# Kernel tuning notes

Measured on AMD Instinct MI355X. Metric: run time of the kernel, lower is better.

## Reference

```python
import jax, jax.numpy as jnp
import numpy as np

B, L, D = 8, 4096, 1024


def setup_inputs() -> dict:
    key = jax.random.key(0)
    k1, k2, k3 = jax.random.split(key, 3)
    scale = 1.0 / np.sqrt(D)  # ~xavier magnitude for DxD
    return {
        "x": jax.random.normal(k1, (B, L, D), dtype=jnp.float32),
        "hidden": jnp.zeros((B, D), dtype=jnp.float32),
        "Wg": jax.random.normal(k2, (D, D), dtype=jnp.float32) * scale,
        "bg": jnp.ones((D,), dtype=jnp.float32),  # gate bias init = 1.0
        "Wh": jax.random.normal(k3, (D, D), dtype=jnp.float32) * scale,
        "bh": jnp.zeros((D,), dtype=jnp.float32),
    }


def reference(x, hidden, Wg, bg, Wh, bh):
    # g_t = sigmoid(x W_g^T + b_g); c_t = tanh(x W_h^T + b_h)
    g = jax.nn.sigmoid(jnp.einsum('bld,ed->ble', x, Wg) + bg)
    c = jnp.tanh(jnp.einsum('bld,ed->ble', x, Wh) + bh)
    # linear recurrence h_t = a_t * h_{t-1} + b_t with a=g, b=(1-g)*c
    a = g
    b = (1.0 - g) * c

    def combine(left, right):
        al, bl = left
        ar, br = right
        return ar * al, ar * bl + br

    A, Bv = jax.lax.associative_scan(combine, (a, b), axis=1)
    # h_t = A_t * h0 + B_t  (cumulative affine map applied to init hidden)
    return A * hidden[:, None, :] + Bv
```

## Files before the change

### kernel.cpp

```cpp
#include <hip/hip_runtime.h>
#include <hip/hip_bf16.h>
#include <cstdint>


using u16   = unsigned short;
using f32x4 = __attribute__((ext_vector_type(4))) float;
using h16x4 = __attribute__((ext_vector_type(4))) _Float16;
using h16x8 = __attribute__((ext_vector_type(8))) _Float16;

#define M_TOTAL 32768
#define K_DIM   1024
#define E_DIM   1024
#define LCH     32
#define NCH     128

__global__ void prep(const float* __restrict__ x,
                     const float* __restrict__ wg, const float* __restrict__ wh,
                     u16* __restrict__ x16, u16* __restrict__ wg16,
                     u16* __restrict__ wh16) {
    const size_t XQ = (size_t)M_TOTAL * K_DIM / 4;
    const size_t WQ = (size_t)K_DIM * E_DIM / 4;
    size_t i = (size_t)blockIdx.x * 256 + threadIdx.x;
    const float* src;
    u16* dst;
    size_t j;
    if (i < XQ)           { src = x;  dst = x16;  j = i; }
    else if (i < XQ + WQ) { src = wg; dst = wg16; j = i - XQ; }
    else                  { src = wh; dst = wh16; j = i - XQ - WQ; }
    f32x4 f = ((const f32x4*)src)[j];
    h16x4 h;
#pragma unroll
    for (int c = 0; c < 4; ++c) h[c] = (_Float16)f[c];
    ((h16x4*)dst)[j] = h;
}

__device__ inline float fast_sigmoid(float z) {
    return 1.f / (1.f + __expf(-z));
}
__device__ inline float fast_tanh(float z) {
    return 1.f - 2.f / (__expf(2.f * z) + 1.f);
}

__global__ __launch_bounds__(512, 4) void gemm_act(
    const u16* __restrict__ x16,
    const u16* __restrict__ wg_h, const u16* __restrict__ wh_h,
    const float* __restrict__ bg, const float* __restrict__ bh,
    _Float16* __restrict__ g_out, _Float16* __restrict__ c_out,
    float* __restrict__ Ac, float* __restrict__ Bc) {

    const int bid   = blockIdx.x;
    const int xcd   = bid & 7;
    const int local = bid >> 3;
    const int mt    = xcd * 32 + (local >> 3);
    const int et    = local & 7;
    const int e0    = et * 128;
    const int m0    = mt * 128;

    __shared__ __align__(16) union SM {
        struct {
            u16 A[512 * 8];
            u16 B[2][512 * 8];
        } buf[2];
        struct {
            float g[32][132];
            float c[32][132];
        } ep;
    } sm;

    const int tid  = threadIdx.x;
    const int lane = tid & 63;
    const int wave = tid >> 6;
    const int wr = wave >> 2, wc = wave & 3;
    const int lr = lane & 15;
    const int kg = lane >> 4;

    const int sp   = tid >> 3;
    const int sc   = tid & 7;
    const int sclog = sc ^ (sp & 7);
    const int srow  = sp * 2 + (sclog >> 2);
    const int skc   = sclog & 3;
    const u16* aSrc = x16 + (size_t)(m0 + srow) * K_DIM + skc * 8;
    const u16* bgSrc = wg_h + (size_t)(e0 + srow) * K_DIM + skc * 8;
    const u16* bhSrc = wh_h + (size_t)(e0 + srow) * K_DIM + skc * 8;

    int aoff[4], boff[2];
#pragma unroll
    for (int tr = 0; tr < 4; ++tr) {
        int r = wr * 64 + tr * 16 + lr;
        int p = r >> 1;
        int c = (((r & 1) << 2) | kg) ^ (p & 7);
        aoff[tr] = p * 64 + c * 8;
    }
#pragma unroll
    for (int tc = 0; tc < 2; ++tc) {
        int e = wc * 32 + tc * 16 + lr;
        int p = e >> 1;
        int c = (((e & 1) << 2) | kg) ^ (p & 7);
        boff[tc] = p * 64 + c * 8;
    }

    f32x4 accg[4][2], acch[4][2];
#pragma unroll
    for (int tr = 0; tr < 4; ++tr)
#pragma unroll
        for (int tc = 0; tc < 2; ++tc) {
            accg[tr][tc] = (f32x4){0.f, 0.f, 0.f, 0.f};
            acch[tr][tc] = (f32x4){0.f, 0.f, 0.f, 0.f};
        }

#define STAGE(bi, kt)                                                          \
    do {                                                                       \
        size_t ko = (size_t)(kt) * 32;                                         \
        __builtin_amdgcn_global_load_lds(                                      \
            (const __attribute__((address_space(1))) void*)(aSrc + ko),        \
            (__attribute__((address_space(3))) void*)(&sm.buf[bi].A[tid * 8]), \
            16, 0, 0);                                                         \
        __builtin_amdgcn_global_load_lds(                                      \
            (const __attribute__((address_space(1))) void*)(bgSrc + ko),       \
            (__attribute__((address_space(3))) void*)(&sm.buf[bi].B[0][tid * 8]),\
            16, 0, 0);                                                         \
        __builtin_amdgcn_global_load_lds(                                      \
            (const __attribute__((address_space(1))) void*)(bhSrc + ko),       \
            (__attribute__((address_space(3))) void*)(&sm.buf[bi].B[1][tid * 8]),\
            16, 0, 0);                                                         \
    } while (0)

    STAGE(0, 0);
    __syncthreads();

    int cur = 0;
    for (int kt = 0; kt < K_DIM / 32; ++kt) {
        if (kt + 1 < K_DIM / 32) STAGE(cur ^ 1, kt + 1);

        const u16* Ab  = sm.buf[cur].A;
        const u16* Bg  = sm.buf[cur].B[0];
        const u16* Bh  = sm.buf[cur].B[1];

        h16x8 ah[4];
#pragma unroll
        for (int tr = 0; tr < 4; ++tr)
            ah[tr] = *(const h16x8*)&Ab[aoff[tr]];
#pragma unroll
        for (int tc = 0; tc < 2; ++tc) {
            h16x8 bgv = *(const h16x8*)&Bg[boff[tc]];
            h16x8 bhv = *(const h16x8*)&Bh[boff[tc]];
#pragma unroll
            for (int tr = 0; tr < 4; ++tr) {
                accg[tr][tc] = __builtin_amdgcn_mfma_f32_16x16x32_f16(ah[tr], bgv, accg[tr][tc], 0, 0, 0);
                acch[tr][tc] = __builtin_amdgcn_mfma_f32_16x16x32_f16(ah[tr], bhv, acch[tr][tc], 0, 0, 0);
            }
        }

        __syncthreads();
        cur ^= 1;
    }
#undef STAGE

    float bgv[2], bhv[2];
#pragma unroll
    for (int tc = 0; tc < 2; ++tc) {
        int el = e0 + wc * 32 + tc * 16 + lr;
        bgv[tc] = bg[el];
        bhv[tc] = bh[el];
    }

#pragma unroll
    for (int s = 0; s < 4; ++s) {
        __syncthreads();
        if (wr == (s >> 1)) {
#pragma unroll
            for (int half = 0; half < 2; ++half) {
                int tr = (s & 1) * 2 + half;
#pragma unroll
                for (int tc = 0; tc < 2; ++tc) {
                    int el = wc * 32 + tc * 16 + lr;
#pragma unroll
                    for (int i = 0; i < 4; ++i) {
                        int row = half * 16 + kg * 4 + i;
                        sm.ep.g[row][el] = fast_sigmoid(accg[tr][tc][i] + bgv[tc]);
                        sm.ep.c[row][el] = fast_tanh(acch[tr][tc][i] + bhv[tc]);
                    }
                }
            }
        }
        __syncthreads();

        {
            int row = tid >> 4;
            int c8  = (tid & 15) * 8;
            size_t gofs = (size_t)(m0 + s * 32 + row) * E_DIM + e0 + c8;
            f32x4 v0 = *(const f32x4*)&sm.ep.g[row][c8];
            f32x4 v1 = *(const f32x4*)&sm.ep.g[row][c8 + 4];
            h16x8 hv;
#pragma unroll
            for (int j = 0; j < 4; ++j) { hv[j] = (_Float16)v0[j]; hv[j + 4] = (_Float16)v1[j]; }
            *(h16x8*)(g_out + gofs) = hv;
            v0 = *(const f32x4*)&sm.ep.c[row][c8];
            v1 = *(const f32x4*)&sm.ep.c[row][c8 + 4];
#pragma unroll
            for (int j = 0; j < 4; ++j) { hv[j] = (_Float16)v0[j]; hv[j + 4] = (_Float16)v1[j]; }
            *(h16x8*)(c_out + gofs) = hv;
        }

        if (tid < 128) {
            float A = 1.f, Bv = 0.f;
#pragma unroll 8
            for (int t = 0; t < LCH; ++t) {
                float g = (float)(_Float16)sm.ep.g[t][tid];
                float c = (float)(_Float16)sm.ep.c[t][tid];
                A  = g * A;
                Bv = g * Bv + (1.f - g) * c;
            }
            int m_abs = m0 + s * 32;
            int b  = m_abs >> 12;
            int ch = (m_abs & 4095) >> 5;
            size_t o = ((size_t)b * NCH + ch) * 1024 + e0 + tid;
            Ac[o] = A;
            Bc[o] = Bv;
        }
    }
}

__global__ void chunk_prefix(const float* __restrict__ Ac, const float* __restrict__ Bc,
                             const float* __restrict__ hidden, float* __restrict__ Hst) {
    int idx = blockIdx.x * 256 + threadIdx.x;
    int b = idx >> 10;
    int d = idx & 1023;
    float h = hidden[b * 1024 + d];
#pragma unroll 8
    for (int ch = 0; ch < NCH; ++ch) {
        size_t o = ((size_t)b * NCH + ch) * 1024 + d;
        float A = Ac[o], Bv = Bc[o];
        Hst[o] = h;
        h = A * h + Bv;
    }
}

__global__ void chunk_apply(const _Float16* __restrict__ g_arr,
                            const _Float16* __restrict__ c_arr,
                            const float* __restrict__ Hst,
                            float* __restrict__ out) {
    int d8 = threadIdx.x * 8;
    int ch = blockIdx.x;
    int b  = blockIdx.y;
    size_t base = ((size_t)b * 4096 + (size_t)ch * LCH) * 1024 + d8;
    size_t ho = ((size_t)b * NCH + ch) * 1024 + d8;
    f32x4 h0 = *(const f32x4*)(Hst + ho);
    f32x4 h1 = *(const f32x4*)(Hst + ho + 4);
    float h[8] = {h0[0], h0[1], h0[2], h0[3], h1[0], h1[1], h1[2], h1[3]};
#pragma unroll 4
    for (int t = 0; t < LCH; ++t) {
        size_t idx = base + (size_t)t * 1024;
        h16x8 gv = *(const h16x8*)(g_arr + idx);
        h16x8 cv = *(const h16x8*)(c_arr + idx);
#pragma unroll
        for (int j = 0; j < 8; ++j) {
            float g = (float)gv[j];
            float c = (float)cv[j];
            h[j] = g * h[j] + (1.f - g) * c;
        }
        *(f32x4*)(out + idx)     = (f32x4){h[0], h[1], h[2], h[3]};
        *(f32x4*)(out + idx + 4) = (f32x4){h[4], h[5], h[6], h[7]};
    }
}

extern "C" void kernel_launch(void* const* d_in, const int* in_sizes, int n_in,
                              void* d_out, int out_size, void* d_ws, size_t ws_size,
                              hipStream_t stream) {
    const float* x      = (const float*)d_in[0];
    const float* hidden = (const float*)d_in[1];
    const float* Wg     = (const float*)d_in[2];
    const float* bg     = (const float*)d_in[3];
    const float* Wh     = (const float*)d_in[4];
    const float* bh     = (const float*)d_in[5];
    float* out = (float*)d_out;

    char* ws = (char*)d_ws;
    const size_t WSEG = 2u * 1024u * 1024u;
    u16* wg_h = (u16*)(ws + 0 * WSEG);
    u16* wh_h = (u16*)(ws + 1 * WSEG);
    const size_t HBYTES = (size_t)M_TOTAL * E_DIM * 2;
    _Float16* g_arr = (_Float16*)(ws + 4 * WSEG);
    _Float16* c_arr = (_Float16*)(ws + 4 * WSEG + HBYTES);
    const size_t SSEG = (size_t)8 * NCH * 1024 * 4;
    float* Ac  = (float*)(ws + 4 * WSEG + 2 * HBYTES);
    float* Bc  = (float*)(ws + 4 * WSEG + 2 * HBYTES + SSEG);
    float* Hst = (float*)(ws + 4 * WSEG + 2 * HBYTES + 2 * SSEG);

    u16* x16 = (u16*)d_out;

    const int XQ = M_TOTAL * (K_DIM / 4);
    const int WQ = K_DIM * (E_DIM / 4);
    prep<<<dim3((XQ + 2 * WQ) / 256), 256, 0, stream>>>(x, Wg, Wh, x16, wg_h, wh_h);

    gemm_act<<<dim3(2048), 512, 0, stream>>>(
        x16, wg_h, wh_h, bg, bh, g_arr, c_arr, Ac, Bc);

    chunk_prefix<<<dim3(32), 256, 0, stream>>>(Ac, Bc, hidden, Hst);
    chunk_apply<<<dim3(NCH, 8), 128, 0, stream>>>(g_arr, c_arr, Hst, out);
}
```

Before: 458.1 us.

## Load GEMM B operands directly from global, grid-stride prep, wider chunk_apply blocks

The GEMM kernel stops staging the Wg/Wh weight tiles through LDS and has each lane load its B fragments straight from global memory every k-step, keeping only the x tile double-buffered in LDS. The aim is to cut LDS traffic and footprint so more blocks fit per CU. The prep conversion kernel becomes a grid-stride loop over 2048 blocks, and chunk_apply handles two chunks per 256-thread block. The risk is that the direct global weight loads are uncoalesced, sit on the critical path without prefetch, and are re-read by every wave instead of being shared through LDS.

```diff
diff --git a/kernel.cpp b/kernel.cpp
--- a/kernel.cpp
+++ b/kernel.cpp
@@ -20,18 +20,21 @@
                      u16* __restrict__ wh16) {
     const size_t XQ = (size_t)M_TOTAL * K_DIM / 4;
     const size_t WQ = (size_t)K_DIM * E_DIM / 4;
-    size_t i = (size_t)blockIdx.x * 256 + threadIdx.x;
-    const float* src;
-    u16* dst;
-    size_t j;
-    if (i < XQ)           { src = x;  dst = x16;  j = i; }
-    else if (i < XQ + WQ) { src = wg; dst = wg16; j = i - XQ; }
-    else                  { src = wh; dst = wh16; j = i - XQ - WQ; }
-    f32x4 f = ((const f32x4*)src)[j];
-    h16x4 h;
-#pragma unroll
-    for (int c = 0; c < 4; ++c) h[c] = (_Float16)f[c];
-    ((h16x4*)dst)[j] = h;
+    const size_t TOT = XQ + 2 * WQ;
+    for (size_t i = (size_t)blockIdx.x * 256 + threadIdx.x; i < TOT;
+         i += (size_t)2048 * 256) {
+        const float* src;
+        u16* dst;
+        size_t j;
+        if (i < XQ)           { src = x;  dst = x16;  j = i; }
+        else if (i < XQ + WQ) { src = wg; dst = wg16; j = i - XQ; }
+        else                  { src = wh; dst = wh16; j = i - XQ - WQ; }
+        f32x4 f = ((const f32x4*)src)[j];
+        h16x4 h;
+#pragma unroll
+        for (int c = 0; c < 4; ++c) h[c] = (_Float16)f[c];
+        ((h16x4*)dst)[j] = h;
+    }
 }
 
 __device__ inline float fast_sigmoid(float z) {
@@ -58,9 +61,8 @@
 
     __shared__ __align__(16) union SM {
         struct {
-            u16 A[512 * 8];
-            u16 B[2][512 * 8];
-        } buf[2];
+            u16 A[2][512 * 8];
+        } s;
         struct {
             float g[32][132];
             float c[32][132];
@@ -74,16 +76,14 @@
     const int lr = lane & 15;
     const int kg = lane >> 4;
 
-    const int sp   = tid >> 3;
-    const int sc   = tid & 7;
+    const int sp    = tid >> 3;
+    const int sc    = tid & 7;
     const int sclog = sc ^ (sp & 7);
     const int srow  = sp * 2 + (sclog >> 2);
     const int skc   = sclog & 3;
     const u16* aSrc = x16 + (size_t)(m0 + srow) * K_DIM + skc * 8;
-    const u16* bgSrc = wg_h + (size_t)(e0 + srow) * K_DIM + skc * 8;
-    const u16* bhSrc = wh_h + (size_t)(e0 + srow) * K_DIM + skc * 8;
-
-    int aoff[4], boff[2];
+
+    int aoff[4];
 #pragma unroll
     for (int tr = 0; tr < 4; ++tr) {
         int r = wr * 64 + tr * 16 + lr;
@@ -91,13 +91,11 @@
         int c = (((r & 1) << 2) | kg) ^ (p & 7);
         aoff[tr] = p * 64 + c * 8;
     }
-#pragma unroll
-    for (int tc = 0; tc < 2; ++tc) {
-        int e = wc * 32 + tc * 16 + lr;
-        int p = e >> 1;
-        int c = (((e & 1) << 2) | kg) ^ (p & 7);
-        boff[tc] = p * 64 + c * 8;
-    }
+
+    size_t eoff[2];
+#pragma unroll
+    for (int tc = 0; tc < 2; ++tc)
+        eoff[tc] = (size_t)(e0 + wc * 32 + tc * 16 + lr) * K_DIM + kg * 8;
 
     f32x4 accg[4][2], acch[4][2];
 #pragma unroll
@@ -108,53 +106,45 @@
             acch[tr][tc] = (f32x4){0.f, 0.f, 0.f, 0.f};
         }
 
-#define STAGE(bi, kt)                                                          \
-    do {                                                                       \
-        size_t ko = (size_t)(kt) * 32;                                         \
-        __builtin_amdgcn_global_load_lds(                                      \
-            (const __attribute__((address_space(1))) void*)(aSrc + ko),        \
-            (__attribute__((address_space(3))) void*)(&sm.buf[bi].A[tid * 8]), \
-            16, 0, 0);                                                         \
-        __builtin_amdgcn_global_load_lds(                                      \
-            (const __attribute__((address_space(1))) void*)(bgSrc + ko),       \
-            (__attribute__((address_space(3))) void*)(&sm.buf[bi].B[0][tid * 8]),\
-            16, 0, 0);                                                         \
-        __builtin_amdgcn_global_load_lds(                                      \
-            (const __attribute__((address_space(1))) void*)(bhSrc + ko),       \
-            (__attribute__((address_space(3))) void*)(&sm.buf[bi].B[1][tid * 8]),\
-            16, 0, 0);                                                         \
-    } while (0)
-
-    STAGE(0, 0);
+#define STAGE_A(bi, kt)                                                        \
+    __builtin_amdgcn_global_load_lds(                                          \
+        (const __attribute__((address_space(1))) void*)(aSrc + (size_t)(kt) * 32),\
+        (__attribute__((address_space(3))) void*)(&sm.s.A[bi][tid * 8]), 16, 0, 0)
+
+    STAGE_A(0, 0);
     __syncthreads();
 
     int cur = 0;
     for (int kt = 0; kt < K_DIM / 32; ++kt) {
-        if (kt + 1 < K_DIM / 32) STAGE(cur ^ 1, kt + 1);
-
-        const u16* Ab  = sm.buf[cur].A;
-        const u16* Bg  = sm.buf[cur].B[0];
-        const u16* Bh  = sm.buf[cur].B[1];
-
+        if (kt + 1 < K_DIM / 32) STAGE_A(cur ^ 1, kt + 1);
+
+        const size_t ko = (size_t)kt * 32;
+        h16x8 bgv0 = *(const h16x8*)(wg_h + eoff[0] + ko);
+        h16x8 bhv0 = *(const h16x8*)(wh_h + eoff[0] + ko);
+        h16x8 bgv1 = *(const h16x8*)(wg_h + eoff[1] + ko);
+        h16x8 bhv1 = *(const h16x8*)(wh_h + eoff[1] + ko);
+
+        const u16* Ab = sm.s.A[cur];
         h16x8 ah[4];
 #pragma unroll
         for (int tr = 0; tr < 4; ++tr)
             ah[tr] = *(const h16x8*)&Ab[aoff[tr]];
-#pragma unroll
-        for (int tc = 0; tc < 2; ++tc) {
-            h16x8 bgv = *(const h16x8*)&Bg[boff[tc]];
-            h16x8 bhv = *(const h16x8*)&Bh[boff[tc]];
-#pragma unroll
-            for (int tr = 0; tr < 4; ++tr) {
-                accg[tr][tc] = __builtin_amdgcn_mfma_f32_16x16x32_f16(ah[tr], bgv, accg[tr][tc], 0, 0, 0);
-                acch[tr][tc] = __builtin_amdgcn_mfma_f32_16x16x32_f16(ah[tr], bhv, acch[tr][tc], 0, 0, 0);
-            }
+
+#pragma unroll
+        for (int tr = 0; tr < 4; ++tr) {
+            accg[tr][0] = __builtin_amdgcn_mfma_f32_16x16x32_f16(ah[tr], bgv0, accg[tr][0], 0, 0, 0);
+            acch[tr][0] = __builtin_amdgcn_mfma_f32_16x16x32_f16(ah[tr], bhv0, acch[tr][0], 0, 0, 0);
+        }
+#pragma unroll
+        for (int tr = 0; tr < 4; ++tr) {
+            accg[tr][1] = __builtin_amdgcn_mfma_f32_16x16x32_f16(ah[tr], bgv1, accg[tr][1], 0, 0, 0);
+            acch[tr][1] = __builtin_amdgcn_mfma_f32_16x16x32_f16(ah[tr], bhv1, acch[tr][1], 0, 0, 0);
         }
 
         __syncthreads();
         cur ^= 1;
     }
-#undef STAGE
+#undef STAGE_A
 
     float bgv[2], bhv[2];
 #pragma unroll
@@ -240,8 +230,9 @@
                             const _Float16* __restrict__ c_arr,
                             const float* __restrict__ Hst,
                             float* __restrict__ out) {
-    int d8 = threadIdx.x * 8;
-    int ch = blockIdx.x;
+    int half = threadIdx.x >> 7;
+    int d8   = (threadIdx.x & 127) * 8;
+    int ch = blockIdx.x * 2 + half;
     int b  = blockIdx.y;
     size_t base = ((size_t)b * 4096 + (size_t)ch * LCH) * 1024 + d8;
     size_t ho = ((size_t)b * NCH + ch) * 1024 + d8;
@@ -289,13 +280,11 @@
 
     u16* x16 = (u16*)d_out;
 
-    const int XQ = M_TOTAL * (K_DIM / 4);
-    const int WQ = K_DIM * (E_DIM / 4);
-    prep<<<dim3((XQ + 2 * WQ) / 256), 256, 0, stream>>>(x, Wg, Wh, x16, wg_h, wh_h);
+    prep<<<dim3(2048), 256, 0, stream>>>(x, Wg, Wh, x16, wg_h, wh_h);
 
     gemm_act<<<dim3(2048), 512, 0, stream>>>(
         x16, wg_h, wh_h, bg, bh, g_arr, c_arr, Ac, Bc);
 
     chunk_prefix<<<dim3(32), 256, 0, stream>>>(Ac, Bc, hidden, Hst);
-    chunk_apply<<<dim3(NCH, 8), 128, 0, stream>>>(g_arr, c_arr, Hst, out);
-}
+    chunk_apply<<<dim3(NCH / 2, 8), 256, 0, stream>>>(g_arr, c_arr, Hst, out);
+}
```

Result: slower. 565.6 us (+23.5%).

## Deepen GEMM load pipeline with vmcnt waits, setprio, grid-stride prep and wider apply blocks

Applied to the files above, without the earlier changes.

The GEMM main loop now issues two stages ahead and waits with explicit s_waitcnt vmcnt(3) and raw barriers instead of __syncthreads after each tile, so global-to-LDS loads overlap MFMA work more. MFMA sections are wrapped in s_setprio to favour compute waves. The prep kernel becomes a grid-stride loop over 2048 blocks, and chunk_apply processes two chunks per 256-thread block. The hand-tuned waitcnt relies on exact load counts per stage and risks races if the compiler reorders memory ops.

```diff
diff --git a/kernel.cpp b/kernel.cpp
--- a/kernel.cpp
+++ b/kernel.cpp
@@ -20,18 +20,21 @@
                      u16* __restrict__ wh16) {
     const size_t XQ = (size_t)M_TOTAL * K_DIM / 4;
     const size_t WQ = (size_t)K_DIM * E_DIM / 4;
-    size_t i = (size_t)blockIdx.x * 256 + threadIdx.x;
-    const float* src;
-    u16* dst;
-    size_t j;
-    if (i < XQ)           { src = x;  dst = x16;  j = i; }
-    else if (i < XQ + WQ) { src = wg; dst = wg16; j = i - XQ; }
-    else                  { src = wh; dst = wh16; j = i - XQ - WQ; }
-    f32x4 f = ((const f32x4*)src)[j];
-    h16x4 h;
-#pragma unroll
-    for (int c = 0; c < 4; ++c) h[c] = (_Float16)f[c];
-    ((h16x4*)dst)[j] = h;
+    const size_t TOT = XQ + 2 * WQ;
+    for (size_t i = (size_t)blockIdx.x * 256 + threadIdx.x; i < TOT;
+         i += (size_t)2048 * 256) {
+        const float* src;
+        u16* dst;
+        size_t j;
+        if (i < XQ)           { src = x;  dst = x16;  j = i; }
+        else if (i < XQ + WQ) { src = wg; dst = wg16; j = i - XQ; }
+        else                  { src = wh; dst = wh16; j = i - XQ - WQ; }
+        f32x4 f = ((const f32x4*)src)[j];
+        h16x4 h;
+#pragma unroll
+        for (int c = 0; c < 4; ++c) h[c] = (_Float16)f[c];
+        ((h16x4*)dst)[j] = h;
+    }
 }
 
 __device__ inline float fast_sigmoid(float z) {
@@ -74,12 +77,12 @@
     const int lr = lane & 15;
     const int kg = lane >> 4;
 
-    const int sp   = tid >> 3;
-    const int sc   = tid & 7;
+    const int sp    = tid >> 3;
+    const int sc    = tid & 7;
     const int sclog = sc ^ (sp & 7);
     const int srow  = sp * 2 + (sclog >> 2);
     const int skc   = sclog & 3;
-    const u16* aSrc = x16 + (size_t)(m0 + srow) * K_DIM + skc * 8;
+    const u16* aSrc  = x16  + (size_t)(m0 + srow) * K_DIM + skc * 8;
     const u16* bgSrc = wg_h + (size_t)(e0 + srow) * K_DIM + skc * 8;
     const u16* bhSrc = wh_h + (size_t)(e0 + srow) * K_DIM + skc * 8;
 
@@ -125,36 +128,50 @@
             16, 0, 0);                                                         \
     } while (0)
 
+#define PHASE(bi)                                                              \
+    do {                                                                       \
+        const u16* Ab = sm.buf[bi].A;                                          \
+        const u16* Bg = sm.buf[bi].B[0];                                       \
+        const u16* Bh = sm.buf[bi].B[1];                                       \
+        h16x8 ah[4];                                                           \
+        _Pragma("unroll")                                                      \
+        for (int tr = 0; tr < 4; ++tr)                                         \
+            ah[tr] = *(const h16x8*)&Ab[aoff[tr]];                             \
+        h16x8 bgv0 = *(const h16x8*)&Bg[boff[0]];                              \
+        h16x8 bhv0 = *(const h16x8*)&Bh[boff[0]];                              \
+        h16x8 bgv1 = *(const h16x8*)&Bg[boff[1]];                              \
+        h16x8 bhv1 = *(const h16x8*)&Bh[boff[1]];                              \
+        __builtin_amdgcn_s_setprio(1);                                         \
+        _Pragma("unroll")                                                      \
+        for (int tr = 0; tr < 4; ++tr) {                                       \
+            accg[tr][0] = __builtin_amdgcn_mfma_f32_16x16x32_f16(ah[tr], bgv0, accg[tr][0], 0, 0, 0); \
+            acch[tr][0] = __builtin_amdgcn_mfma_f32_16x16x32_f16(ah[tr], bhv0, acch[tr][0], 0, 0, 0); \
+        }                                                                      \
+        _Pragma("unroll")                                                      \
+        for (int tr = 0; tr < 4; ++tr) {                                       \
+            accg[tr][1] = __builtin_amdgcn_mfma_f32_16x16x32_f16(ah[tr], bgv1, accg[tr][1], 0, 0, 0); \
+            acch[tr][1] = __builtin_amdgcn_mfma_f32_16x16x32_f16(ah[tr], bhv1, acch[tr][1], 0, 0, 0); \
+        }                                                                      \
+        __builtin_amdgcn_s_setprio(0);                                         \
+    } while (0)
+
     STAGE(0, 0);
-    __syncthreads();
+    STAGE(1, 1);
 
     int cur = 0;
-    for (int kt = 0; kt < K_DIM / 32; ++kt) {
-        if (kt + 1 < K_DIM / 32) STAGE(cur ^ 1, kt + 1);
-
-        const u16* Ab  = sm.buf[cur].A;
-        const u16* Bg  = sm.buf[cur].B[0];
-        const u16* Bh  = sm.buf[cur].B[1];
-
-        h16x8 ah[4];
-#pragma unroll
-        for (int tr = 0; tr < 4; ++tr)
-            ah[tr] = *(const h16x8*)&Ab[aoff[tr]];
-#pragma unroll
-        for (int tc = 0; tc < 2; ++tc) {
-            h16x8 bgv = *(const h16x8*)&Bg[boff[tc]];
-            h16x8 bhv = *(const h16x8*)&Bh[boff[tc]];
-#pragma unroll
-            for (int tr = 0; tr < 4; ++tr) {
-                accg[tr][tc] = __builtin_amdgcn_mfma_f32_16x16x32_f16(ah[tr], bgv, accg[tr][tc], 0, 0, 0);
-                acch[tr][tc] = __builtin_amdgcn_mfma_f32_16x16x32_f16(ah[tr], bhv, acch[tr][tc], 0, 0, 0);
-            }
-        }
-
-        __syncthreads();
+    for (int kt = 0; kt < 31; ++kt) {
+        asm volatile("s_waitcnt vmcnt(3)" ::: "memory");
+        __builtin_amdgcn_s_barrier();
+        PHASE(cur);
+        __builtin_amdgcn_s_barrier();
+        if (kt < 30) STAGE(cur, kt + 2);
         cur ^= 1;
     }
+    asm volatile("s_waitcnt vmcnt(0)" ::: "memory");
+    __builtin_amdgcn_s_barrier();
+    PHASE(cur);
 #undef STAGE
+#undef PHASE
 
     float bgv[2], bhv[2];
 #pragma unroll
@@ -240,8 +257,9 @@
                             const _Float16* __restrict__ c_arr,
                             const float* __restrict__ Hst,
                             float* __restrict__ out) {
-    int d8 = threadIdx.x * 8;
-    int ch = blockIdx.x;
+    int half = threadIdx.x >> 7;
+    int d8   = (threadIdx.x & 127) * 8;
+    int ch = blockIdx.x * 2 + half;
     int b  = blockIdx.y;
     size_t base = ((size_t)b * 4096 + (size_t)ch * LCH) * 1024 + d8;
     size_t ho = ((size_t)b * NCH + ch) * 1024 + d8;
@@ -289,13 +307,11 @@
 
     u16* x16 = (u16*)d_out;
 
-    const int XQ = M_TOTAL * (K_DIM / 4);
-    const int WQ = K_DIM * (E_DIM / 4);
-    prep<<<dim3((XQ + 2 * WQ) / 256), 256, 0, stream>>>(x, Wg, Wh, x16, wg_h, wh_h);
+    prep<<<dim3(2048), 256, 0, stream>>>(x, Wg, Wh, x16, wg_h, wh_h);
 
     gemm_act<<<dim3(2048), 512, 0, stream>>>(
         x16, wg_h, wh_h, bg, bh, g_arr, c_arr, Ac, Bc);
 
     chunk_prefix<<<dim3(32), 256, 0, stream>>>(Ac, Bc, hidden, Hst);
-    chunk_apply<<<dim3(NCH, 8), 128, 0, stream>>>(g_arr, c_arr, Hst, out);
-}
+    chunk_apply<<<dim3(NCH / 2, 8), 256, 0, stream>>>(g_arr, c_arr, Hst, out);
+}
```

New measurement: 457.6 us. Within noise of the previous version (-0.1%).

## Enlarge per-wave GEMM tiles, triple-buffer LDS with vmcnt waits, reshape prep and apply

Applied to the files above, without the earlier changes.

The GEMM kernel drops from 512 to 256 threads, so each wave now computes a 64x64 output tile per gate instead of 64x32. This raises register-level reuse of the A fragments and cuts LDS reads per MFMA. The K loop moves from double to triple buffering: explicit vmcnt waits and a single barrier per iteration replace two __syncthreads, and s_setprio is raised around the MFMA block. prep becomes a grid-stride loop over a fixed grid, and chunk_apply handles two chunks per 256-thread block. The trade-off is higher LDS use (72KB per block) and more accumulator registers, which may limit occupancy.

```diff
diff --git a/kernel.cpp b/kernel.cpp
--- a/kernel.cpp
+++ b/kernel.cpp
@@ -20,18 +20,21 @@
                      u16* __restrict__ wh16) {
     const size_t XQ = (size_t)M_TOTAL * K_DIM / 4;
     const size_t WQ = (size_t)K_DIM * E_DIM / 4;
-    size_t i = (size_t)blockIdx.x * 256 + threadIdx.x;
-    const float* src;
-    u16* dst;
-    size_t j;
-    if (i < XQ)           { src = x;  dst = x16;  j = i; }
-    else if (i < XQ + WQ) { src = wg; dst = wg16; j = i - XQ; }
-    else                  { src = wh; dst = wh16; j = i - XQ - WQ; }
-    f32x4 f = ((const f32x4*)src)[j];
-    h16x4 h;
-#pragma unroll
-    for (int c = 0; c < 4; ++c) h[c] = (_Float16)f[c];
-    ((h16x4*)dst)[j] = h;
+    const size_t TOT = XQ + 2 * WQ;
+    for (size_t i = (size_t)blockIdx.x * 256 + threadIdx.x; i < TOT;
+         i += (size_t)2048 * 256) {
+        const float* src;
+        u16* dst;
+        size_t j;
+        if (i < XQ)           { src = x;  dst = x16;  j = i; }
+        else if (i < XQ + WQ) { src = wg; dst = wg16; j = i - XQ; }
+        else                  { src = wh; dst = wh16; j = i - XQ - WQ; }
+        f32x4 f = ((const f32x4*)src)[j];
+        h16x4 h;
+#pragma unroll
+        for (int c = 0; c < 4; ++c) h[c] = (_Float16)f[c];
+        ((h16x4*)dst)[j] = h;
+    }
 }
 
 __device__ inline float fast_sigmoid(float z) {
@@ -41,7 +44,7 @@
     return 1.f - 2.f / (__expf(2.f * z) + 1.f);
 }
 
-__global__ __launch_bounds__(512, 4) void gemm_act(
+__global__ __launch_bounds__(256, 2) void gemm_act(
     const u16* __restrict__ x16,
     const u16* __restrict__ wg_h, const u16* __restrict__ wh_h,
     const float* __restrict__ bg, const float* __restrict__ bh,
@@ -60,7 +63,7 @@
         struct {
             u16 A[512 * 8];
             u16 B[2][512 * 8];
-        } buf[2];
+        } buf[3];
         struct {
             float g[32][132];
             float c[32][132];
@@ -70,20 +73,24 @@
     const int tid  = threadIdx.x;
     const int lane = tid & 63;
     const int wave = tid >> 6;
-    const int wr = wave >> 2, wc = wave & 3;
+    const int wr = wave >> 1, wc = wave & 1;
     const int lr = lane & 15;
     const int kg = lane >> 4;
 
-    const int sp   = tid >> 3;
-    const int sc   = tid & 7;
-    const int sclog = sc ^ (sp & 7);
-    const int srow  = sp * 2 + (sclog >> 2);
-    const int skc   = sclog & 3;
-    const u16* aSrc = x16 + (size_t)(m0 + srow) * K_DIM + skc * 8;
-    const u16* bgSrc = wg_h + (size_t)(e0 + srow) * K_DIM + skc * 8;
-    const u16* bhSrc = wh_h + (size_t)(e0 + srow) * K_DIM + skc * 8;
-
-    int aoff[4], boff[2];
+    size_t aO[2], wO[2];
+#pragma unroll
+    for (int j = 0; j < 2; ++j) {
+        int ch    = tid + 256 * j;
+        int p     = ch >> 3;
+        int c     = ch & 7;
+        int clog  = c ^ (p & 7);
+        int row   = p * 2 + (clog >> 2);
+        int kc    = clog & 3;
+        aO[j] = (size_t)(m0 + row) * K_DIM + kc * 8;
+        wO[j] = (size_t)(e0 + row) * K_DIM + kc * 8;
+    }
+
+    int aoff[4], boff[4];
 #pragma unroll
     for (int tr = 0; tr < 4; ++tr) {
         int r = wr * 64 + tr * 16 + lr;
@@ -92,18 +99,18 @@
         aoff[tr] = p * 64 + c * 8;
     }
 #pragma unroll
-    for (int tc = 0; tc < 2; ++tc) {
-        int e = wc * 32 + tc * 16 + lr;
+    for (int tc = 0; tc < 4; ++tc) {
+        int e = wc * 64 + tc * 16 + lr;
         int p = e >> 1;
         int c = (((e & 1) << 2) | kg) ^ (p & 7);
         boff[tc] = p * 64 + c * 8;
     }
 
-    f32x4 accg[4][2], acch[4][2];
+    f32x4 accg[4][4], acch[4][4];
 #pragma unroll
     for (int tr = 0; tr < 4; ++tr)
 #pragma unroll
-        for (int tc = 0; tc < 2; ++tc) {
+        for (int tc = 0; tc < 4; ++tc) {
             accg[tr][tc] = (f32x4){0.f, 0.f, 0.f, 0.f};
             acch[tr][tc] = (f32x4){0.f, 0.f, 0.f, 0.f};
         }
@@ -111,37 +118,43 @@
 #define STAGE(bi, kt)                                                          \
     do {                                                                       \
         size_t ko = (size_t)(kt) * 32;                                         \
-        __builtin_amdgcn_global_load_lds(                                      \
-            (const __attribute__((address_space(1))) void*)(aSrc + ko),        \
-            (__attribute__((address_space(3))) void*)(&sm.buf[bi].A[tid * 8]), \
-            16, 0, 0);                                                         \
-        __builtin_amdgcn_global_load_lds(                                      \
-            (const __attribute__((address_space(1))) void*)(bgSrc + ko),       \
-            (__attribute__((address_space(3))) void*)(&sm.buf[bi].B[0][tid * 8]),\
-            16, 0, 0);                                                         \
-        __builtin_amdgcn_global_load_lds(                                      \
-            (const __attribute__((address_space(1))) void*)(bhSrc + ko),       \
-            (__attribute__((address_space(3))) void*)(&sm.buf[bi].B[1][tid * 8]),\
-            16, 0, 0);                                                         \
+        _Pragma("unroll")                                                      \
+        for (int j = 0; j < 2; ++j) {                                          \
+            __builtin_amdgcn_global_load_lds(                                  \
+                (const __attribute__((address_space(1))) void*)(x16 + aO[j] + ko),\
+                (__attribute__((address_space(3))) void*)(&sm.buf[bi].A[(tid + 256 * j) * 8]),\
+                16, 0, 0);                                                     \
+            __builtin_amdgcn_global_load_lds(                                  \
+                (const __attribute__((address_space(1))) void*)(wg_h + wO[j] + ko),\
+                (__attribute__((address_space(3))) void*)(&sm.buf[bi].B[0][(tid + 256 * j) * 8]),\
+                16, 0, 0);                                                     \
+            __builtin_amdgcn_global_load_lds(                                  \
+                (const __attribute__((address_space(1))) void*)(wh_h + wO[j] + ko),\
+                (__attribute__((address_space(3))) void*)(&sm.buf[bi].B[1][(tid + 256 * j) * 8]),\
+                16, 0, 0);                                                     \
+        }                                                                      \
     } while (0)
 
     STAGE(0, 0);
-    __syncthreads();
-
-    int cur = 0;
-    for (int kt = 0; kt < K_DIM / 32; ++kt) {
-        if (kt + 1 < K_DIM / 32) STAGE(cur ^ 1, kt + 1);
-
-        const u16* Ab  = sm.buf[cur].A;
-        const u16* Bg  = sm.buf[cur].B[0];
-        const u16* Bh  = sm.buf[cur].B[1];
-
+    STAGE(1, 1);
+
+    for (int kt = 0; kt < 32; ++kt) {
+        if (kt < 31) asm volatile("s_waitcnt vmcnt(6)" ::: "memory");
+        else         asm volatile("s_waitcnt vmcnt(0)" ::: "memory");
+        __builtin_amdgcn_s_barrier();
+        if (kt < 30) STAGE((kt + 2) % 3, kt + 2);
+
+        const int bi = kt % 3;
+        const u16* Ab = sm.buf[bi].A;
+        const u16* Bg = sm.buf[bi].B[0];
+        const u16* Bh = sm.buf[bi].B[1];
         h16x8 ah[4];
 #pragma unroll
         for (int tr = 0; tr < 4; ++tr)
             ah[tr] = *(const h16x8*)&Ab[aoff[tr]];
-#pragma unroll
-        for (int tc = 0; tc < 2; ++tc) {
+        __builtin_amdgcn_s_setprio(1);
+#pragma unroll
+        for (int tc = 0; tc < 4; ++tc) {
             h16x8 bgv = *(const h16x8*)&Bg[boff[tc]];
             h16x8 bhv = *(const h16x8*)&Bh[boff[tc]];
 #pragma unroll
@@ -150,16 +163,14 @@
                 acch[tr][tc] = __builtin_amdgcn_mfma_f32_16x16x32_f16(ah[tr], bhv, acch[tr][tc], 0, 0, 0);
             }
         }
-
-        __syncthreads();
-        cur ^= 1;
+        __builtin_amdgcn_s_setprio(0);
     }
 #undef STAGE
 
-    float bgv[2], bhv[2];
-#pragma unroll
-    for (int tc = 0; tc < 2; ++tc) {
-        int el = e0 + wc * 32 + tc * 16 + lr;
+    float bgv[4], bhv[4];
+#pragma unroll
+    for (int tc = 0; tc < 4; ++tc) {
+        int el = e0 + wc * 64 + tc * 16 + lr;
         bgv[tc] = bg[el];
         bhv[tc] = bh[el];
     }
@@ -172,8 +183,8 @@
             for (int half = 0; half < 2; ++half) {
                 int tr = (s & 1) * 2 + half;
 #pragma unroll
-                for (int tc = 0; tc < 2; ++tc) {
-                    int el = wc * 32 + tc * 16 + lr;
+                for (int tc = 0; tc < 4; ++tc) {
+                    int el = wc * 64 + tc * 16 + lr;
 #pragma unroll
                     for (int i = 0; i < 4; ++i) {
                         int row = half * 16 + kg * 4 + i;
@@ -185,8 +196,9 @@
         }
         __syncthreads();
 
-        {
-            int row = tid >> 4;
+#pragma unroll
+        for (int p = 0; p < 2; ++p) {
+            int row = p * 16 + (tid >> 4);
             int c8  = (tid & 15) * 8;
             size_t gofs = (size_t)(m0 + s * 32 + row) * E_DIM + e0 + c8;
             f32x4 v0 = *(const f32x4*)&sm.ep.g[row][c8];
@@ -240,8 +252,9 @@
                             const _Float16* __restrict__ c_arr,
                             const float* __restrict__ Hst,
                             float* __restrict__ out) {
-    int d8 = threadIdx.x * 8;
-    int ch = blockIdx.x;
+    int half = threadIdx.x >> 7;
+    int d8   = (threadIdx.x & 127) * 8;
+    int ch = blockIdx.x * 2 + half;
     int b  = blockIdx.y;
     size_t base = ((size_t)b * 4096 + (size_t)ch * LCH) * 1024 + d8;
     size_t ho = ((size_t)b * NCH + ch) * 1024 + d8;
@@ -289,13 +302,11 @@
 
     u16* x16 = (u16*)d_out;
 
-    const int XQ = M_TOTAL * (K_DIM / 4);
-    const int WQ = K_DIM * (E_DIM / 4);
-    prep<<<dim3((XQ + 2 * WQ) / 256), 256, 0, stream>>>(x, Wg, Wh, x16, wg_h, wh_h);
-
-    gemm_act<<<dim3(2048), 512, 0, stream>>>(
+    prep<<<dim3(2048), 256, 0, stream>>>(x, Wg, Wh, x16, wg_h, wh_h);
+
+    gemm_act<<<dim3(2048), 256, 0, stream>>>(
         x16, wg_h, wh_h, bg, bh, g_arr, c_arr, Ac, Bc);
 
     chunk_prefix<<<dim3(32), 256, 0, stream>>>(Ac, Bc, hidden, Hst);
-    chunk_apply<<<dim3(NCH, 8), 128, 0, stream>>>(g_arr, c_arr, Hst, out);
-}
+    chunk_apply<<<dim3(NCH / 2, 8), 256, 0, stream>>>(g_arr, c_arr, Hst, out);
+}
```

After: 477.2 us. 1.04x slower.
